# Optimization experiments

Measured on AMD Instinct MI355X. Metric: run time of the kernel, lower is better.

## Reference

```python
import jax, jax.numpy as jnp
import numpy as np

N, E, CIN, HOPS, HID, COUT = 50000, 800000, 64, 3, 256, 64

def setup_inputs() -> dict:
    key = jax.random.key(0)
    ks = jax.random.split(key, 8)
    x = jax.random.normal(ks[0], (N, CIN), dtype=jnp.float32)
    edge_index = jax.random.randint(ks[1], (2, E), 0, N, dtype=jnp.int64)
    def lin(k, fan_in, fan_out):
        bound = 1.0 / np.sqrt(fan_in)
        return jax.random.uniform(k, (fan_in, fan_out), jnp.float32, -bound, bound)
    W0 = lin(ks[2], CIN * (HOPS + 1), HID)
    W1 = lin(ks[3], HID, HID)
    W2 = lin(ks[4], HID, COUT)
    b0 = jnp.zeros((HID,), jnp.float32)
    b1 = jnp.zeros((HID,), jnp.float32)
    b2 = jnp.zeros((COUT,), jnp.float32)
    return {"x": x, "edge_index": edge_index, "W0": W0, "b0": b0, "W1": W1, "b1": b1, "W2": W2, "b2": b2}

def reference(x, edge_index, W0, b0, W1, b1, W2, b2):
    row, col = edge_index[0], edge_index[1]
    n = x.shape[0]
    # degree of destination nodes (degree(col, N))
    d = jax.ops.segment_sum(jnp.ones_like(col, dtype=jnp.float32), col, num_segments=n)
    d_norm_in = 1.0 / jnp.sqrt(d[col])   # per-edge
    d_norm_out = 1.0 / jnp.sqrt(d[row])
    value = d_norm_in * d_norm_out
    value = jnp.where(jnp.isfinite(value), value, 0.0)  # nan_to_num
    def spmm(h):
        # adj has entries at (col[e], row[e]) -> out[i] = sum_{e: col[e]=i} value[e] * h[row[e]]
        return jax.ops.segment_sum(value[:, None] * h[row], col, num_segments=n)
    emb = [x]
    h = x
    for _ in range(HOPS):
        h = spmm(h)
        emb.append(h)
    z = jnp.concatenate(emb, axis=1)  # [N, CIN*(HOPS+1)]
    # eval mode: dropout is identity, use_bn=False
    z = jax.nn.relu(z @ W0 + b0)
    z = jax.nn.relu(z @ W1 + b1)
    return z @ W2 + b2
```

## Files before the change

kernel.cpp:

```cpp
#include <hip/hip_runtime.h>


#define ZW 256
#define NCH 64

typedef __attribute__((ext_vector_type(8))) __bf16 bf16x8;
typedef __attribute__((ext_vector_type(4))) float f32x4;

__device__ __forceinline__ unsigned f2bf(float f) {
    unsigned x = __float_as_uint(f);
    return (x + 0x7fffu + ((x >> 16) & 1u)) >> 16;
}
__device__ __forceinline__ unsigned pack_split(float v) {
    unsigned hb = f2bf(v);
    float hf = __uint_as_float(hb << 16);
    unsigned lb = f2bf(v - hf);
    return (hb << 16) | lb;
}
__device__ __forceinline__ float unpack_f(unsigned u) {
    return __uint_as_float(u & 0xffff0000u) + __uint_as_float(u << 16);
}

__device__ __forceinline__ void gload16(const void* g, void* l) {
    __builtin_amdgcn_global_load_lds(
        (const __attribute__((address_space(1))) unsigned*)g,
        (__attribute__((address_space(3))) unsigned*)l, 16, 0, 0);
}


__global__ void init_kernel(const float* __restrict__ x, unsigned* __restrict__ zp,
                            int* __restrict__ deg, int N) {
    int stride = gridDim.x * blockDim.x;
    int total4 = N * 16;
    for (int idx = blockIdx.x * blockDim.x + threadIdx.x; idx < total4; idx += stride) {
        int n = idx >> 4, c4 = idx & 15;
        float4 v = *reinterpret_cast<const float4*>(x + (size_t)n * NCH + c4 * 4);
        uint4 o;
        o.x = pack_split(v.x); o.y = pack_split(v.y);
        o.z = pack_split(v.z); o.w = pack_split(v.w);
        *reinterpret_cast<uint4*>(zp + (size_t)n * ZW + c4 * 4) = o;
    }
    for (int idx = blockIdx.x * blockDim.x + threadIdx.x; idx < N; idx += stride)
        deg[idx] = 0;
}

__global__ void degree_kernel(const int* __restrict__ col, int* __restrict__ deg,
                              int E, int N) {
    int slice = blockIdx.x & 7;
    int g = blockIdx.x >> 3;
    int G = gridDim.x >> 3;
    int sliceN = (N + 7) >> 3;
    int lo = slice * sliceN;
    int hi = lo + sliceN; if (hi > N) hi = N;
    int stride = G * blockDim.x;
    for (int e = g * blockDim.x + threadIdx.x; e < E; e += stride) {
        int c = col[e];
        if (c >= lo && c < hi) atomicAdd(&deg[c], 1);
    }
}

__global__ __launch_bounds__(1024) void scan_part_kernel(const int* __restrict__ deg,
                                                         int* __restrict__ off,
                                                         int* __restrict__ bsum, int N) {
    __shared__ int smem[1024];
    int tid = threadIdx.x;
    int i = blockIdx.x * 1024 + tid;
    int v = (i < N) ? deg[i] : 0;
    smem[tid] = v;
    __syncthreads();
    for (int o = 1; o < 1024; o <<= 1) {
        int t = (tid >= o) ? smem[tid - o] : 0;
        __syncthreads();
        smem[tid] += t;
        __syncthreads();
    }
    if (i < N) off[i] = smem[tid] - v;
    if (tid == 1023) bsum[blockIdx.x] = smem[1023];
}

__global__ void scan_tops_kernel(const int* __restrict__ bsum, int* __restrict__ btot, int nb) {
    int lane = threadIdx.x;
    int v = (lane < nb) ? bsum[lane] : 0;
    int incl = v;
    for (int o = 1; o < 64; o <<= 1) {
        int t = __shfl_up(incl, o);
        if (lane >= o) incl += t;
    }
    if (lane < nb) btot[lane] = incl - v;
    if (lane == 63) btot[nb] = incl;
}

__global__ __launch_bounds__(1024) void scan_add_kernel(int* __restrict__ off,
                                                        int* __restrict__ cur,
                                                        const int* __restrict__ btot,
                                                        int N, int nb) {
    int i = blockIdx.x * 1024 + threadIdx.x;
    if (i < N) {
        int o = off[i] + btot[blockIdx.x];
        off[i] = o;
        cur[i] = o;
    }
    if (i == 0) off[N] = btot[nb];
}

__global__ void scatter_kernel(const int* __restrict__ row, const int* __restrict__ col,
                               const int* __restrict__ deg, int* __restrict__ cursor,
                               int2* __restrict__ meta, int E, int N) {
    int slice = blockIdx.x & 7;
    int g = blockIdx.x >> 3;
    int G = gridDim.x >> 3;
    int sliceN = (N + 7) >> 3;
    int lo = slice * sliceN;
    int hi = lo + sliceN; if (hi > N) hi = N;
    int stride = G * blockDim.x;
    for (int e = g * blockDim.x + threadIdx.x; e < E; e += stride) {
        int c = col[e];
        if (c >= lo && c < hi) {
            int r = row[e];
            int dc = deg[c];
            int dr = deg[r];
            float v = 0.0f;
            if (dc > 0 && dr > 0) v = rsqrtf((float)dc * (float)dr);
            int pos = atomicAdd(&cursor[c], 1);
            meta[pos] = make_int2(r, __float_as_int(v));
        }
    }
}

__global__ void spmm_csr_kernel(const int* __restrict__ offsets, const int2* __restrict__ meta,
                                const unsigned* __restrict__ zin, unsigned* __restrict__ zout,
                                int N) {
    int lane = threadIdx.x & 63;
    int wave = (blockIdx.x * blockDim.x + threadIdx.x) >> 6;
    if (wave >= N) return;
    int start = offsets[wave];
    int end   = offsets[wave + 1];
    float acc = 0.0f;
    int j = start;
    for (; j + 4 <= end; j += 4) {
        int2 m0 = meta[j];
        int2 m1 = meta[j + 1];
        int2 m2 = meta[j + 2];
        int2 m3 = meta[j + 3];
        float h0 = unpack_f(zin[(size_t)m0.x * ZW + lane]);
        float h1 = unpack_f(zin[(size_t)m1.x * ZW + lane]);
        float h2 = unpack_f(zin[(size_t)m2.x * ZW + lane]);
        float h3 = unpack_f(zin[(size_t)m3.x * ZW + lane]);
        acc = fmaf(__int_as_float(m0.y), h0, acc);
        acc = fmaf(__int_as_float(m1.y), h1, acc);
        acc = fmaf(__int_as_float(m2.y), h2, acc);
        acc = fmaf(__int_as_float(m3.y), h3, acc);
    }
    for (; j + 2 <= end; j += 2) {
        int2 m0 = meta[j];
        int2 m1 = meta[j + 1];
        float h0 = unpack_f(zin[(size_t)m0.x * ZW + lane]);
        float h1 = unpack_f(zin[(size_t)m1.x * ZW + lane]);
        acc = fmaf(__int_as_float(m0.y), h0, acc);
        acc = fmaf(__int_as_float(m1.y), h1, acc);
    }
    if (j < end) {
        int2 m0 = meta[j];
        acc = fmaf(__int_as_float(m0.y), unpack_f(zin[(size_t)m0.x * ZW + lane]), acc);
    }
    zout[(size_t)wave * ZW + lane] = pack_split(acc);
}

__global__ void prep_w_kernel(const float* __restrict__ W0, const float* __restrict__ W1,
                              const float* __restrict__ W2, unsigned short* __restrict__ ws) {
    int idx = blockIdx.x * blockDim.x + threadIdx.x;
    if (idx >= 65536) return;
    int n = idx >> 8, k = idx & 255;
    unsigned p0 = pack_split(W0[(size_t)k * 256 + n]);
    ws[idx]          = (unsigned short)(p0 >> 16);
    ws[65536 + idx]  = (unsigned short)(p0 & 0xffff);
    unsigned p1 = pack_split(W1[(size_t)k * 256 + n]);
    ws[131072 + idx] = (unsigned short)(p1 >> 16);
    ws[196608 + idx] = (unsigned short)(p1 & 0xffff);
    if (idx < 16384) {
        int n2 = idx >> 8, k2 = idx & 255;
        unsigned p2 = pack_split(W2[(size_t)k2 * 64 + n2]);
        ws[262144 + idx] = (unsigned short)(p2 >> 16);
        ws[278528 + idx] = (unsigned short)(p2 & 0xffff);
    }
}

__global__ __launch_bounds__(256, 2) void gemm256_kernel(
        const unsigned* __restrict__ Ap, const unsigned short* __restrict__ Wh,
        const unsigned short* __restrict__ Wl, const float* __restrict__ bias,
        unsigned* __restrict__ Cp, int M) {
    __shared__ unsigned Apl[2 * 128 * 32];
    __shared__ unsigned short Bhl[2 * 128 * 32];
    __shared__ unsigned short Bll[2 * 128 * 32];

    int tid = threadIdx.x;
    int lane = tid & 63;
    int wid = tid >> 6;
    int wr = wid >> 1, wc = wid & 1;
    int bm = blockIdx.x * 128;
    int bn = blockIdx.y * 128;
    int l15 = lane & 15, kg = lane >> 4;

    f32x4 acc[4][4] = {};

    auto STAGE = [&](int buf, int k0) {
        unsigned* Ab = Apl + buf * (128 * 32);
        unsigned short* Bhb = Bhl + buf * (128 * 32);
        unsigned short* Blb = Bll + buf * (128 * 32);
#pragma unroll
        for (int i = 0; i < 4; ++i) {
            int s = (wid * 4 + i) * 64 + lane;
            int r = s >> 3, cp = s & 7;
            int cl = cp ^ (r & 7);
            int grow = bm + r; if (grow >= M) grow = M - 1;
            gload16(Ap + (size_t)grow * 256 + k0 + cl * 4, Ab + (wid * 4 + i) * 256);
        }
#pragma unroll
        for (int i = 0; i < 2; ++i) {
            int s = (wid * 2 + i) * 64 + lane;
            int n = s >> 2, cp = s & 3;
            int cl = cp ^ ((n >> 1) & 3);
            size_t goff = (size_t)(bn + n) * 256 + k0 + cl * 8;
            gload16(Wh + goff, Bhb + (wid * 2 + i) * 512);
            gload16(Wl + goff, Blb + (wid * 2 + i) * 512);
        }
    };

    auto COMPUTE = [&](int buf) {
        const unsigned* Ab = Apl + buf * (128 * 32);
        const unsigned short* Bhb = Bhl + buf * (128 * 32);
        const unsigned short* Blb = Bll + buf * (128 * 32);
        bf16x8 bh[4], bl[4];
#pragma unroll
        for (int n4 = 0; n4 < 4; ++n4) {
            int nn = wc * 64 + n4 * 16 + l15;
            int c = kg ^ ((nn >> 1) & 3);
            bh[n4] = *reinterpret_cast<const bf16x8*>(&Bhb[nn * 32 + c * 8]);
            bl[n4] = *reinterpret_cast<const bf16x8*>(&Blb[nn * 32 + c * 8]);
        }
#pragma unroll
        for (int m = 0; m < 4; ++m) {
            int r = wr * 64 + m * 16 + l15;
            int c0 = (2 * kg) ^ (r & 7);
            int c1 = (2 * kg + 1) ^ (r & 7);
            uint4 q0 = *reinterpret_cast<const uint4*>(&Ab[r * 32 + c0 * 4]);
            uint4 q1 = *reinterpret_cast<const uint4*>(&Ab[r * 32 + c1 * 4]);
            union { bf16x8 v; unsigned short s[8]; } ah, al;
            ah.s[0] = (unsigned short)(q0.x >> 16); al.s[0] = (unsigned short)q0.x;
            ah.s[1] = (unsigned short)(q0.y >> 16); al.s[1] = (unsigned short)q0.y;
            ah.s[2] = (unsigned short)(q0.z >> 16); al.s[2] = (unsigned short)q0.z;
            ah.s[3] = (unsigned short)(q0.w >> 16); al.s[3] = (unsigned short)q0.w;
            ah.s[4] = (unsigned short)(q1.x >> 16); al.s[4] = (unsigned short)q1.x;
            ah.s[5] = (unsigned short)(q1.y >> 16); al.s[5] = (unsigned short)q1.y;
            ah.s[6] = (unsigned short)(q1.z >> 16); al.s[6] = (unsigned short)q1.z;
            ah.s[7] = (unsigned short)(q1.w >> 16); al.s[7] = (unsigned short)q1.w;
#pragma unroll
            for (int n4 = 0; n4 < 4; ++n4) {
                acc[m][n4] = __builtin_amdgcn_mfma_f32_16x16x32_bf16(ah.v, bh[n4], acc[m][n4], 0, 0, 0);
                acc[m][n4] = __builtin_amdgcn_mfma_f32_16x16x32_bf16(ah.v, bl[n4], acc[m][n4], 0, 0, 0);
                acc[m][n4] = __builtin_amdgcn_mfma_f32_16x16x32_bf16(al.v, bh[n4], acc[m][n4], 0, 0, 0);
            }
        }
    };

    STAGE(0, 0);
    __syncthreads();
#pragma unroll
    for (int t = 0; t < 8; ++t) {
        if (t < 7) STAGE((t + 1) & 1, (t + 1) * 32);
        COMPUTE(t & 1);
        __syncthreads();
    }

#pragma unroll
    for (int n4 = 0; n4 < 4; ++n4) {
        int col = bn + wc * 64 + n4 * 16 + l15;
        float bv = bias[col];
#pragma unroll
        for (int m = 0; m < 4; ++m) {
#pragma unroll
            for (int rr = 0; rr < 4; ++rr) {
                int row = bm + wr * 64 + m * 16 + kg * 4 + rr;
                if (row < M) {
                    float v = fmaxf(acc[m][n4][rr] + bv, 0.0f);
                    Cp[(size_t)row * 256 + col] = pack_split(v);
                }
            }
        }
    }
}

__global__ __launch_bounds__(256, 3) void gemm64_kernel(
        const unsigned* __restrict__ Ap, const unsigned short* __restrict__ Wh,
        const unsigned short* __restrict__ Wl, const float* __restrict__ bias,
        float* __restrict__ out, int M) {
    __shared__ unsigned Apl[2 * 128 * 32];
    __shared__ unsigned short Bhl[2 * 64 * 32];
    __shared__ unsigned short Bll[2 * 64 * 32];

    int tid = threadIdx.x;
    int lane = tid & 63;
    int wid = tid >> 6;
    int bm = blockIdx.x * 128;
    int l15 = lane & 15, kg = lane >> 4;

    f32x4 acc[2][4] = {};

    auto STAGE = [&](int buf, int k0) {
        unsigned* Ab = Apl + buf * (128 * 32);
        unsigned short* Bhb = Bhl + buf * (64 * 32);
        unsigned short* Blb = Bll + buf * (64 * 32);
#pragma unroll
        for (int i = 0; i < 4; ++i) {
            int s = (wid * 4 + i) * 64 + lane;
            int r = s >> 3, cp = s & 7;
            int cl = cp ^ (r & 7);
            int grow = bm + r; if (grow >= M) grow = M - 1;
            gload16(Ap + (size_t)grow * 256 + k0 + cl * 4, Ab + (wid * 4 + i) * 256);
        }
        {
            int s = wid * 64 + lane;
            int n = s >> 2, cp = s & 3;
            int cl = cp ^ ((n >> 1) & 3);
            size_t goff = (size_t)n * 256 + k0 + cl * 8;
            gload16(Wh + goff, Bhb + wid * 512);
            gload16(Wl + goff, Blb + wid * 512);
        }
    };

    auto COMPUTE = [&](int buf) {
        const unsigned* Ab = Apl + buf * (128 * 32);
        const unsigned short* Bhb = Bhl + buf * (64 * 32);
        const unsigned short* Blb = Bll + buf * (64 * 32);
        bf16x8 bh[4], bl[4];
#pragma unroll
        for (int n4 = 0; n4 < 4; ++n4) {
            int nn = n4 * 16 + l15;
            int c = kg ^ ((nn >> 1) & 3);
            bh[n4] = *reinterpret_cast<const bf16x8*>(&Bhb[nn * 32 + c * 8]);
            bl[n4] = *reinterpret_cast<const bf16x8*>(&Blb[nn * 32 + c * 8]);
        }
#pragma unroll
        for (int m = 0; m < 2; ++m) {
            int r = wid * 32 + m * 16 + l15;
            int c0 = (2 * kg) ^ (r & 7);
            int c1 = (2 * kg + 1) ^ (r & 7);
            uint4 q0 = *reinterpret_cast<const uint4*>(&Ab[r * 32 + c0 * 4]);
            uint4 q1 = *reinterpret_cast<const uint4*>(&Ab[r * 32 + c1 * 4]);
            union { bf16x8 v; unsigned short s[8]; } ah, al;
            ah.s[0] = (unsigned short)(q0.x >> 16); al.s[0] = (unsigned short)q0.x;
            ah.s[1] = (unsigned short)(q0.y >> 16); al.s[1] = (unsigned short)q0.y;
            ah.s[2] = (unsigned short)(q0.z >> 16); al.s[2] = (unsigned short)q0.z;
            ah.s[3] = (unsigned short)(q0.w >> 16); al.s[3] = (unsigned short)q0.w;
            ah.s[4] = (unsigned short)(q1.x >> 16); al.s[4] = (unsigned short)q1.x;
            ah.s[5] = (unsigned short)(q1.y >> 16); al.s[5] = (unsigned short)q1.y;
            ah.s[6] = (unsigned short)(q1.z >> 16); al.s[6] = (unsigned short)q1.z;
            ah.s[7] = (unsigned short)(q1.w >> 16); al.s[7] = (unsigned short)q1.w;
#pragma unroll
            for (int n4 = 0; n4 < 4; ++n4) {
                acc[m][n4] = __builtin_amdgcn_mfma_f32_16x16x32_bf16(ah.v, bh[n4], acc[m][n4], 0, 0, 0);
                acc[m][n4] = __builtin_amdgcn_mfma_f32_16x16x32_bf16(ah.v, bl[n4], acc[m][n4], 0, 0, 0);
                acc[m][n4] = __builtin_amdgcn_mfma_f32_16x16x32_bf16(al.v, bh[n4], acc[m][n4], 0, 0, 0);
            }
        }
    };

    STAGE(0, 0);
    __syncthreads();
#pragma unroll
    for (int t = 0; t < 8; ++t) {
        if (t < 7) STAGE((t + 1) & 1, (t + 1) * 32);
        COMPUTE(t & 1);
        __syncthreads();
    }

#pragma unroll
    for (int n4 = 0; n4 < 4; ++n4) {
        int col = n4 * 16 + l15;
        float bv = bias[col];
#pragma unroll
        for (int m = 0; m < 2; ++m) {
#pragma unroll
            for (int rr = 0; rr < 4; ++rr) {
                int row = bm + wid * 32 + m * 16 + kg * 4 + rr;
                if (row < M) out[(size_t)row * 64 + col] = acc[m][n4][rr] + bv;
            }
        }
    }
}

extern "C" void kernel_launch(void* const* d_in, const int* in_sizes, int n_in,
                              void* d_out, int out_size, void* d_ws, size_t ws_size,
                              hipStream_t stream) {
    const float* x  = (const float*)d_in[0];
    const int* ei   = (const int*)d_in[1];
    const float* W0 = (const float*)d_in[2];
    const float* b0 = (const float*)d_in[3];
    const float* W1 = (const float*)d_in[4];
    const float* b1 = (const float*)d_in[5];
    const float* W2 = (const float*)d_in[6];
    const float* b2 = (const float*)d_in[7];
    float* out = (float*)d_out;

    const int N = in_sizes[0] / NCH;
    const int E = in_sizes[1] / 2;
    const int* row = ei;
    const int* col = ei + E;

    unsigned* zp = (unsigned*)d_ws;
    unsigned* hp = zp + (size_t)N * ZW;
    unsigned short* wsp = (unsigned short*)(hp + (size_t)N * ZW);
    int* deg  = (int*)(wsp + 294912);
    int* off  = deg + N;
    int* cur  = off + N + 1;
    int* bsum = cur + N;
    int* btot = bsum + 64;
    int2* meta = (int2*)hp;

    const int TB = 256;
    const int NB = (N + 1023) / 1024;

    prep_w_kernel<<<256, TB, 0, stream>>>(W0, W1, W2, wsp);
    init_kernel<<<2048, TB, 0, stream>>>(x, zp, deg, N);
    degree_kernel<<<1024, TB, 0, stream>>>(col, deg, E, N);
    scan_part_kernel<<<NB, 1024, 0, stream>>>(deg, off, bsum, N);
    scan_tops_kernel<<<1, 64, 0, stream>>>(bsum, btot, NB);
    scan_add_kernel<<<NB, 1024, 0, stream>>>(off, cur, btot, N, NB);
    scatter_kernel<<<1024, TB, 0, stream>>>(row, col, deg, cur, meta, E, N);

    int spmm_blocks = (N * 64 + TB - 1) / TB;
    for (int hop = 1; hop <= 3; ++hop) {
        const unsigned* zin = zp + (hop - 1) * NCH;
        unsigned* zout      = zp + hop * NCH;
        spmm_csr_kernel<<<spmm_blocks, TB, 0, stream>>>(off, meta, zin, zout, N);
    }

    int gblocks = (N + 127) / 128;
    dim3 g256(gblocks, 2);
    gemm256_kernel<<<g256, TB, 0, stream>>>(zp, wsp,          wsp + 65536,  b0, hp, N);
    gemm256_kernel<<<g256, TB, 0, stream>>>(hp, wsp + 131072, wsp + 196608, b1, zp, N);
    gemm64_kernel<<<gblocks, TB, 0, stream>>>(zp, wsp + 262144, wsp + 278528, b2, out, N);
}
```

Measured before the change: 381.4 us.

## Load weight fragments directly from global memory and pipeline A staging with vmcnt waits

Both GEMM kernels stop staging the split-bf16 weight tiles through LDS and instead load the B fragments straight from global memory (expected to hit L2/L1) inside the compute step. Only the activation tile is still double-buffered in LDS. Explicit s_waitcnt vmcnt and raw s_barrier calls replace __syncthreads so the next A tile's loads stay in flight during compute. The 256-wide GEMM's occupancy hint rises from 2 to 3 blocks per CU because of the freed LDS. The trade-off is that global B loads now sit on the MFMA critical path with uncoalesced 16-byte accesses, and the hand-counted vmcnt must match the in-flight loads, which the new global B loads may disturb.

```diff
diff --git a/kernel.cpp b/kernel.cpp
--- a/kernel.cpp
+++ b/kernel.cpp
@@ -185,13 +185,11 @@
     }
 }
 
-__global__ __launch_bounds__(256, 2) void gemm256_kernel(
+__global__ __launch_bounds__(256, 3) void gemm256_kernel(
         const unsigned* __restrict__ Ap, const unsigned short* __restrict__ Wh,
         const unsigned short* __restrict__ Wl, const float* __restrict__ bias,
         unsigned* __restrict__ Cp, int M) {
     __shared__ unsigned Apl[2 * 128 * 32];
-    __shared__ unsigned short Bhl[2 * 128 * 32];
-    __shared__ unsigned short Bll[2 * 128 * 32];
 
     int tid = threadIdx.x;
     int lane = tid & 63;
@@ -205,8 +203,6 @@
 
     auto STAGE = [&](int buf, int k0) {
         unsigned* Ab = Apl + buf * (128 * 32);
-        unsigned short* Bhb = Bhl + buf * (128 * 32);
-        unsigned short* Blb = Bll + buf * (128 * 32);
 #pragma unroll
         for (int i = 0; i < 4; ++i) {
             int s = (wid * 4 + i) * 64 + lane;
@@ -215,28 +211,17 @@
             int grow = bm + r; if (grow >= M) grow = M - 1;
             gload16(Ap + (size_t)grow * 256 + k0 + cl * 4, Ab + (wid * 4 + i) * 256);
         }
-#pragma unroll
-        for (int i = 0; i < 2; ++i) {
-            int s = (wid * 2 + i) * 64 + lane;
-            int n = s >> 2, cp = s & 3;
-            int cl = cp ^ ((n >> 1) & 3);
-            size_t goff = (size_t)(bn + n) * 256 + k0 + cl * 8;
-            gload16(Wh + goff, Bhb + (wid * 2 + i) * 512);
-            gload16(Wl + goff, Blb + (wid * 2 + i) * 512);
-        }
     };
 
-    auto COMPUTE = [&](int buf) {
+    auto COMPUTE = [&](int buf, int k0) {
         const unsigned* Ab = Apl + buf * (128 * 32);
-        const unsigned short* Bhb = Bhl + buf * (128 * 32);
-        const unsigned short* Blb = Bll + buf * (128 * 32);
         bf16x8 bh[4], bl[4];
 #pragma unroll
         for (int n4 = 0; n4 < 4; ++n4) {
             int nn = wc * 64 + n4 * 16 + l15;
-            int c = kg ^ ((nn >> 1) & 3);
-            bh[n4] = *reinterpret_cast<const bf16x8*>(&Bhb[nn * 32 + c * 8]);
-            bl[n4] = *reinterpret_cast<const bf16x8*>(&Blb[nn * 32 + c * 8]);
+            size_t go = (size_t)(bn + nn) * 256 + k0 + kg * 8;
+            bh[n4] = *reinterpret_cast<const bf16x8*>(Wh + go);
+            bl[n4] = *reinterpret_cast<const bf16x8*>(Wl + go);
         }
 #pragma unroll
         for (int m = 0; m < 4; ++m) {
@@ -264,12 +249,18 @@
     };
 
     STAGE(0, 0);
-    __syncthreads();
 #pragma unroll
     for (int t = 0; t < 8; ++t) {
-        if (t < 7) STAGE((t + 1) & 1, (t + 1) * 32);
-        COMPUTE(t & 1);
-        __syncthreads();
+        if (t < 7) {
+            STAGE((t + 1) & 1, (t + 1) * 32);
+            asm volatile("s_waitcnt vmcnt(4)" ::: "memory");
+        } else {
+            asm volatile("s_waitcnt vmcnt(0)" ::: "memory");
+        }
+        __builtin_amdgcn_s_barrier();
+        COMPUTE(t & 1, t * 32);
+        __builtin_amdgcn_s_barrier();
+        __builtin_amdgcn_sched_barrier(0);
     }
 
 #pragma unroll
@@ -295,8 +286,6 @@
         const unsigned short* __restrict__ Wl, const float* __restrict__ bias,
         float* __restrict__ out, int M) {
     __shared__ unsigned Apl[2 * 128 * 32];
-    __shared__ unsigned short Bhl[2 * 64 * 32];
-    __shared__ unsigned short Bll[2 * 64 * 32];
 
     int tid = threadIdx.x;
     int lane = tid & 63;
@@ -308,8 +297,6 @@
 
     auto STAGE = [&](int buf, int k0) {
         unsigned* Ab = Apl + buf * (128 * 32);
-        unsigned short* Bhb = Bhl + buf * (64 * 32);
-        unsigned short* Blb = Bll + buf * (64 * 32);
 #pragma unroll
         for (int i = 0; i < 4; ++i) {
             int s = (wid * 4 + i) * 64 + lane;
@@ -318,27 +305,17 @@
             int grow = bm + r; if (grow >= M) grow = M - 1;
             gload16(Ap + (size_t)grow * 256 + k0 + cl * 4, Ab + (wid * 4 + i) * 256);
         }
-        {
-            int s = wid * 64 + lane;
-            int n = s >> 2, cp = s & 3;
-            int cl = cp ^ ((n >> 1) & 3);
-            size_t goff = (size_t)n * 256 + k0 + cl * 8;
-            gload16(Wh + goff, Bhb + wid * 512);
-            gload16(Wl + goff, Blb + wid * 512);
-        }
     };
 
-    auto COMPUTE = [&](int buf) {
+    auto COMPUTE = [&](int buf, int k0) {
         const unsigned* Ab = Apl + buf * (128 * 32);
-        const unsigned short* Bhb = Bhl + buf * (64 * 32);
-        const unsigned short* Blb = Bll + buf * (64 * 32);
         bf16x8 bh[4], bl[4];
 #pragma unroll
         for (int n4 = 0; n4 < 4; ++n4) {
             int nn = n4 * 16 + l15;
-            int c = kg ^ ((nn >> 1) & 3);
-            bh[n4] = *reinterpret_cast<const bf16x8*>(&Bhb[nn * 32 + c * 8]);
-            bl[n4] = *reinterpret_cast<const bf16x8*>(&Blb[nn * 32 + c * 8]);
+            size_t go = (size_t)nn * 256 + k0 + kg * 8;
+            bh[n4] = *reinterpret_cast<const bf16x8*>(Wh + go);
+            bl[n4] = *reinterpret_cast<const bf16x8*>(Wl + go);
         }
 #pragma unroll
         for (int m = 0; m < 2; ++m) {
@@ -366,12 +343,18 @@
     };
 
     STAGE(0, 0);
-    __syncthreads();
 #pragma unroll
     for (int t = 0; t < 8; ++t) {
-        if (t < 7) STAGE((t + 1) & 1, (t + 1) * 32);
-        COMPUTE(t & 1);
-        __syncthreads();
+        if (t < 7) {
+            STAGE((t + 1) & 1, (t + 1) * 32);
+            asm volatile("s_waitcnt vmcnt(4)" ::: "memory");
+        } else {
+            asm volatile("s_waitcnt vmcnt(0)" ::: "memory");
+        }
+        __builtin_amdgcn_s_barrier();
+        COMPUTE(t & 1, t * 32);
+        __builtin_amdgcn_s_barrier();
+        __builtin_amdgcn_sched_barrier(0);
     }
 
 #pragma unroll
```

Measured after the change: 417.9 us. +9.6%, slower.
